# Kernel tuning notes

Hardware: AMD Instinct MI355X
Metric: run time of the kernel (lower is better)

## Reference

```python
import jax, jax.numpy as jnp
import numpy as np

B, N, M = 16, 4096, 1024
C2, C1 = 256, 128          # points2 channels (in_channel), points1 channels
MLP = [256, 256]
IN0 = C2 + C1              # use_points1=True concat


def setup_inputs() -> dict:
    key = jax.random.key(0)
    ks = jax.random.split(key, 8)
    inp = {
        "xyz1": jax.random.normal(ks[0], (B, 3, N), jnp.float32),
        "xyz2": jax.random.normal(ks[1], (B, 3, M), jnp.float32),
        "points1": jax.random.normal(ks[2], (B, C1, N), jnp.float32),
        "points2": jax.random.normal(ks[3], (B, C2, M), jnp.float32),
        # 1x1 Conv1d weights == dense matrices (out, in)
        "W1": jax.random.normal(ks[4], (MLP[0], IN0), jnp.float32) / np.sqrt(IN0),
        "b1": jnp.zeros((MLP[0],), jnp.float32),
        "W2": jax.random.normal(ks[5], (MLP[1], MLP[0]), jnp.float32) / np.sqrt(MLP[0]),
        "b2": jnp.zeros((MLP[1],), jnp.float32),
    }
    return inp


def _fp(xyz1, xyz2, points1, points2, W1, b1, W2, b2):
    # three_nn: squared pairwise distances via ||a||^2 + ||b||^2 - 2 a.b
    # xyz*: (B, 3, N/M)
    sq1 = jnp.sum(xyz1 * xyz1, axis=1)                 # (B, N)
    sq2 = jnp.sum(xyz2 * xyz2, axis=1)                 # (B, M)
    inner = jnp.einsum("bcn,bcm->bnm", xyz1, xyz2)     # (B, N, M)
    d2 = sq1[:, :, None] + sq2[:, None, :] - 2.0 * inner
    neg_d2, idx = jax.lax.top_k(-d2, 3)                # 3 smallest -> (B, N, 3)
    dist = jnp.sqrt(jnp.maximum(-neg_d2, 1e-20))       # Euclidean, like three_nn wrapper
    dist = jnp.maximum(dist, 1e-10)                    # torch.clamp_min
    recip = 1.0 / dist
    weight = recip / jnp.sum(recip, axis=2, keepdims=True)  # (B, N, 3)
    # three_interpolate: gather points2 at idx and weighted-sum
    gathered = jax.vmap(lambda p, i: p[:, i])(points2, idx)  # (B, C2, N, 3)
    interp = jnp.einsum("bcnk,bnk->bcn", gathered, weight)   # (B, C2, N)
    x = jnp.concatenate([interp, points1], axis=1)           # (B, C2+C1, N)
    # mlp_conv: 1x1 conv + relu (if_bn=False)
    x = jax.nn.relu(jnp.einsum("oc,bcn->bon", W1, x) + b1[None, :, None])
    x = jax.nn.relu(jnp.einsum("oc,bcn->bon", W2, x) + b2[None, :, None])
    return x


def reference(xyz1, xyz2, points1, points2, W1, b1, W2, b2):
    return _fp(xyz1, xyz2, points1, points2, W1, b1, W2, b2)
```

## Files before the change

### kernel.cpp

```cpp
#include <hip/hip_runtime.h>

#define B_  16
#define N_  4096
#define M_  1024
#define C1_ 128
#define C2_ 256
#define K0_ 384
#define O1_ 256
#define O2_ 256

typedef _Float16 half4  __attribute__((ext_vector_type(4)));
typedef _Float16 half8  __attribute__((ext_vector_type(8)));
typedef float    f32x4  __attribute__((ext_vector_type(4)));

__global__ __launch_bounds__(256)
void three_nn_kernel(const float* __restrict__ xyz1, const float* __restrict__ xyz2,
                     int* __restrict__ idxb, float* __restrict__ wb) {
    __shared__ float pts[4 * 1028];
    int b = blockIdx.y;
    int t = threadIdx.x;
    {
        const float* src = xyz2 + (size_t)b * 3 * M_;
        int m0 = t * 4;
        f32x4 xv = *(const f32x4*)(src + m0);
        f32x4 yv = *(const f32x4*)(src + M_ + m0);
        f32x4 zv = *(const f32x4*)(src + 2 * M_ + m0);
        float* dst = pts + (t >> 6) * 1028 + (m0 & 255) * 4;
#pragma unroll
        for (int jj = 0; jj < 4; ++jj) {
            f32x4 o = {xv[jj], yv[jj], zv[jj],
                       fmaf(xv[jj], xv[jj], fmaf(yv[jj], yv[jj], zv[jj] * zv[jj]))};
            *(f32x4*)(dst + jj * 4) = o;
        }
    }
    __syncthreads();
    int lane = t & 63;
    int c = lane & 3;
    int q = ((t >> 6) << 4) + (lane >> 2);
    int n = blockIdx.x * 64 + q;
    const float* qp = xyz1 + (size_t)b * 3 * N_;
    float px = qp[n], py = qp[N_ + n], pz = qp[2 * N_ + n];
    float px2 = -2.f * px, py2 = -2.f * py, pz2 = -2.f * pz;
    const float* base = pts + c * 1028;
    float b0 = 1e30f, b1v = 1e30f, b2v = 1e30f;
    int i0 = 0, i1 = 0, i2 = 0;
    int mb = c * 256;
#pragma unroll 4
    for (int i = 0; i < 256; ++i) {
        f32x4 pv = *(const f32x4*)(base + i * 4);
        float d = fmaf(pv[0], px2, fmaf(pv[1], py2, fmaf(pv[2], pz2, pv[3])));
        int m = mb + i;
        bool c0 = d < b0, c1 = d < b1v, c2 = d < b2v;
        float nb1 = __builtin_amdgcn_fmed3f(d, b0, b1v);
        float nb2 = __builtin_amdgcn_fmed3f(d, b1v, b2v);
        i2 = c1 ? i1 : (c2 ? m : i2);
        i1 = c0 ? i0 : (c1 ? m : i1);
        i0 = c0 ? m : i0;
        b0 = fminf(b0, d);
        b1v = nb1; b2v = nb2;
    }
#pragma unroll
    for (int st = 1; st <= 2; st <<= 1) {
        float d0 = __shfl_xor(b0, st, 64);  int j0 = __shfl_xor(i0, st, 64);
        float d1 = __shfl_xor(b1v, st, 64); int j1 = __shfl_xor(i1, st, 64);
        float d2 = __shfl_xor(b2v, st, 64); int j2 = __shfl_xor(i2, st, 64);
#pragma unroll
        for (int e = 0; e < 3; ++e) {
            float d = (e == 0) ? d0 : (e == 1) ? d1 : d2;
            int   m = (e == 0) ? j0 : (e == 1) ? j1 : j2;
            bool c0 = d < b0, c1 = d < b1v, c2 = d < b2v;
            float nb1 = __builtin_amdgcn_fmed3f(d, b0, b1v);
            float nb2 = __builtin_amdgcn_fmed3f(d, b1v, b2v);
            i2 = c1 ? i1 : (c2 ? m : i2);
            i1 = c0 ? i0 : (c1 ? m : i1);
            i0 = c0 ? m : i0;
            b0 = fminf(b0, d);
            b1v = nb1; b2v = nb2;
        }
    }
    if (c == 0) {
        float sq1 = fmaf(px, px, fmaf(py, py, pz * pz));
        float e0 = fmaxf(sqrtf(fmaxf(b0 + sq1, 1e-20f)), 1e-10f);
        float e1 = fmaxf(sqrtf(fmaxf(b1v + sq1, 1e-20f)), 1e-10f);
        float e2 = fmaxf(sqrtf(fmaxf(b2v + sq1, 1e-20f)), 1e-10f);
        float r0 = 1.f / e0, r1 = 1.f / e1, r2 = 1.f / e2;
        float s = r0 + r1 + r2;
        size_t j = ((size_t)b * N_ + n) * 3;
        idxb[j] = i0; idxb[j + 1] = i1; idxb[j + 2] = i2;
        wb[j] = r0 / s; wb[j + 1] = r1 / s; wb[j + 2] = r2 / s;
    }
}

__global__ __launch_bounds__(256)
void convert_w_kernel(const float* __restrict__ W1, const float* __restrict__ W2,
                      _Float16* __restrict__ W1h, _Float16* __restrict__ W2h) {
    int t = blockIdx.x * 256 + threadIdx.x;
    if (t < O1_ * K0_) W1h[t] = (_Float16)W1[t];
    if (t < O2_ * O1_) W2h[t] = (_Float16)W2[t];
}

__global__ __launch_bounds__(256)
void transpose_f16_kernel(const float* __restrict__ in, _Float16* __restrict__ out) {
    __shared__ float tile[64][65];
    int t = threadIdx.x;
    int nb = blockIdx.x * 64, cb = blockIdx.y * 64;
    const float* ib = in + (size_t)blockIdx.z * C2_ * M_;
#pragma unroll
    for (int r = 0; r < 16; ++r) {
        int cc = r * 4 + (t >> 6);
        tile[cc][t & 63] = ib[(size_t)(cb + cc) * M_ + nb + (t & 63)];
    }
    __syncthreads();
    _Float16* ob = out + (size_t)blockIdx.z * M_ * C2_;
#pragma unroll
    for (int pass = 0; pass < 2; ++pass) {
        int id = pass * 256 + t;
        int nl = id >> 3;
        int c8 = (id & 7) * 8;
        half8 v;
#pragma unroll
        for (int jj = 0; jj < 8; ++jj) v[jj] = (_Float16)tile[c8 + jj][nl];
        *(half8*)(ob + (size_t)(nb + nl) * C2_ + cb + c8) = v;
    }
}

__global__ __launch_bounds__(256, 2)
void fused_mlp_kernel(const _Float16* __restrict__ p2T, const int* __restrict__ idxb,
                      const float* __restrict__ wb, const float* __restrict__ points1,
                      const _Float16* __restrict__ W1h, const float* __restrict__ b1,
                      const _Float16* __restrict__ W2h, const float* __restrict__ b2,
                      float* __restrict__ out) {
    __shared__ _Float16 Y1s[128 * 256];
    char* ybase = (char*)Y1s;
    int b = blockIdx.y;
    int n0b = blockIdx.x * 128;
    int t = threadIdx.x, lane = t & 63, wv = t >> 6;
    int lr = lane & 15, lh = lane >> 4;
    int wvn = wv >> 1, wvo = wv & 1;
    int swz = (lr & 7) << 4;

    int ia[4], ib_[4], ic[4];
    float wa[4], wbv[4], wcv[4];
    const _Float16* p2b = p2T + (size_t)b * M_ * C2_;
#pragma unroll
    for (int nf = 0; nf < 4; ++nf) {
        int n = n0b + wvn * 64 + nf * 16 + lr;
        size_t j = ((size_t)b * N_ + n) * 3;
        ia[nf] = idxb[j]; ib_[nf] = idxb[j + 1]; ic[nf] = idxb[j + 2];
        wa[nf] = wb[j]; wbv[nf] = wb[j + 1]; wcv[nf] = wb[j + 2];
    }

    f32x4 acc[8][4];
#pragma unroll
    for (int of = 0; of < 8; ++of) {
        int o = wvo * 128 + of * 16 + lh * 4;
        f32x4 bv = {b1[o], b1[o + 1], b1[o + 2], b1[o + 3]};
#pragma unroll
        for (int nf = 0; nf < 4; ++nf) acc[of][nf] = bv;
    }
    const _Float16* w1p = W1h + (size_t)(wvo * 128 + lr) * K0_ + lh * 8;

    for (int k0 = 0; k0 < 256; k0 += 32) {
        half8 bf[4];
#pragma unroll
        for (int nf = 0; nf < 4; ++nf) {
            const _Float16* g0 = p2b + (size_t)ia[nf]  * C2_ + k0 + lh * 8;
            const _Float16* g1 = p2b + (size_t)ib_[nf] * C2_ + k0 + lh * 8;
            const _Float16* g2 = p2b + (size_t)ic[nf]  * C2_ + k0 + lh * 8;
            half8 va = *(const half8*)g0, vb = *(const half8*)g1, vc = *(const half8*)g2;
#pragma unroll
            for (int jj = 0; jj < 8; ++jj) {
                float v = wa[nf] * (float)va[jj] + wbv[nf] * (float)vb[jj]
                        + wcv[nf] * (float)vc[jj];
                bf[nf][jj] = (_Float16)v;
            }
        }
#pragma unroll
        for (int of = 0; of < 8; ++of) {
            half8 af = *(const half8*)(w1p + (size_t)of * 16 * K0_ + k0);
#pragma unroll
            for (int nf = 0; nf < 4; ++nf)
                acc[of][nf] = __builtin_amdgcn_mfma_f32_16x16x32_f16(af, bf[nf], acc[of][nf], 0, 0, 0);
        }
    }
    for (int k0 = 0; k0 < 128; k0 += 32) {
        half8 bf[4];
#pragma unroll
        for (int nf = 0; nf < 4; ++nf) {
            int n = n0b + wvn * 64 + nf * 16 + lr;
            const float* pp = points1 + ((size_t)b * C1_ + k0 + lh * 8) * N_ + n;
#pragma unroll
            for (int jj = 0; jj < 8; ++jj) bf[nf][jj] = (_Float16)pp[(size_t)jj * N_];
        }
#pragma unroll
        for (int of = 0; of < 8; ++of) {
            half8 af = *(const half8*)(w1p + (size_t)of * 16 * K0_ + 256 + k0);
#pragma unroll
            for (int nf = 0; nf < 4; ++nf)
                acc[of][nf] = __builtin_amdgcn_mfma_f32_16x16x32_f16(af, bf[nf], acc[of][nf], 0, 0, 0);
        }
    }
#pragma unroll
    for (int of = 0; of < 8; ++of) {
#pragma unroll
        for (int nf = 0; nf < 4; ++nf) {
            int nloc = wvn * 64 + nf * 16 + lr;
            int obyte = (wvo * 128 + of * 16 + lh * 4) * 2;
            half4 h;
#pragma unroll
            for (int r = 0; r < 4; ++r) h[r] = (_Float16)fmaxf(acc[of][nf][r], 0.f);
            *(half4*)(ybase + ((nloc * 512 + obyte) ^ swz)) = h;
        }
    }
    __syncthreads();

    f32x4 acc2[4][8];
    int o2b = wv * 64;
#pragma unroll
    for (int of = 0; of < 4; ++of) {
        int o = o2b + of * 16 + lh * 4;
        f32x4 bv = {b2[o], b2[o + 1], b2[o + 2], b2[o + 3]};
#pragma unroll
        for (int nf = 0; nf < 8; ++nf) acc2[of][nf] = bv;
    }
    const _Float16* w2p = W2h + (size_t)(o2b + lr) * O1_ + lh * 8;
    for (int k0 = 0; k0 < 256; k0 += 32) {
        half8 av[4];
#pragma unroll
        for (int of = 0; of < 4; ++of) av[of] = *(const half8*)(w2p + (size_t)of * 16 * O1_ + k0);
#pragma unroll
        for (int nf = 0; nf < 8; ++nf) {
            half8 bb = *(const half8*)(ybase + ((((nf * 16 + lr) * 512) + k0 * 2 + lh * 16) ^ swz));
#pragma unroll
            for (int of = 0; of < 4; ++of)
                acc2[of][nf] = __builtin_amdgcn_mfma_f32_16x16x32_f16(av[of], bb, acc2[of][nf], 0, 0, 0);
        }
    }
    float* ob = out + (size_t)b * O2_ * N_;
#pragma unroll
    for (int of = 0; of < 4; ++of) {
#pragma unroll
        for (int r = 0; r < 4; ++r) {
            int o2 = o2b + of * 16 + lh * 4 + r;
#pragma unroll
            for (int nf = 0; nf < 8; ++nf)
                ob[(size_t)o2 * N_ + n0b + nf * 16 + lr] = fmaxf(acc2[of][nf][r], 0.f);
        }
    }
}

extern "C" void kernel_launch(void* const* d_in, const int* in_sizes, int n_in,
                              void* d_out, int out_size, void* d_ws, size_t ws_size,
                              hipStream_t stream) {
    const float* xyz1    = (const float*)d_in[0];
    const float* xyz2    = (const float*)d_in[1];
    const float* points1 = (const float*)d_in[2];
    const float* points2 = (const float*)d_in[3];
    const float* W1      = (const float*)d_in[4];
    const float* b1      = (const float*)d_in[5];
    const float* W2      = (const float*)d_in[6];
    const float* b2      = (const float*)d_in[7];
    float* out = (float*)d_out;

    char* p = (char*)d_ws;
    auto alloc = [&](size_t bytes) -> char* {
        char* r = p;
        p += (bytes + 255) & ~(size_t)255;
        return r;
    };
    _Float16* W1h  = (_Float16*)alloc((size_t)O1_ * K0_ * 2);
    _Float16* W2h  = (_Float16*)alloc((size_t)O2_ * O1_ * 2);
    int*      idxb = (int*)alloc((size_t)B_ * N_ * 3 * 4);
    float*    wbuf = (float*)alloc((size_t)B_ * N_ * 3 * 4);
    _Float16* p2T  = (_Float16*)alloc((size_t)B_ * M_ * C2_ * 2);
    (void)ws_size;

    convert_w_kernel<<<dim3((O1_ * K0_ + 255) / 256), 256, 0, stream>>>(W1, W2, W1h, W2h);
    three_nn_kernel<<<dim3(N_ / 64, B_), 256, 0, stream>>>(xyz1, xyz2, idxb, wbuf);
    transpose_f16_kernel<<<dim3(M_ / 64, C2_ / 64, B_), 256, 0, stream>>>(points2, p2T);
    fused_mlp_kernel<<<dim3(N_ / 128, B_), 256, 0, stream>>>(
        p2T, idxb, wbuf, points1, W1h, b1, W2h, b2, out);
}
```

Measured before the change: 202.5 us.

## Stage interpolated features in LDS, retile MLP to 64-point blocks, pre-transpose points1

The fused MLP kernel now gathers and interpolates the points2 features once into swizzled shared memory, then runs both 1x1-conv GEMMs from LDS. It uses 512-thread blocks over 64 points with smaller per-wave accumulators, which allows higher occupancy. points1 is optionally transposed to fp16 first when the workspace is large enough, so it can be read with vector loads instead of strided scalar loads. three_nn now splits each query across 8 lanes with half the candidate range per lane and runs twice as many blocks. In exchange there is an extra transpose pass over points1 and a larger dynamic shared memory footprint.

```diff
diff --git a/kernel.cpp b/kernel.cpp
--- a/kernel.cpp
+++ b/kernel.cpp
@@ -16,7 +16,7 @@
 __global__ __launch_bounds__(256)
 void three_nn_kernel(const float* __restrict__ xyz1, const float* __restrict__ xyz2,
                      int* __restrict__ idxb, float* __restrict__ wb) {
-    __shared__ float pts[4 * 1028];
+    __shared__ float pts[8 * 516];
     int b = blockIdx.y;
     int t = threadIdx.x;
     {
@@ -25,7 +25,7 @@
         f32x4 xv = *(const f32x4*)(src + m0);
         f32x4 yv = *(const f32x4*)(src + M_ + m0);
         f32x4 zv = *(const f32x4*)(src + 2 * M_ + m0);
-        float* dst = pts + (t >> 6) * 1028 + (m0 & 255) * 4;
+        float* dst = pts + (m0 >> 7) * 516 + (m0 & 127) * 4;
 #pragma unroll
         for (int jj = 0; jj < 4; ++jj) {
             f32x4 o = {xv[jj], yv[jj], zv[jj],
@@ -35,18 +35,18 @@
     }
     __syncthreads();
     int lane = t & 63;
-    int c = lane & 3;
-    int q = ((t >> 6) << 4) + (lane >> 2);
-    int n = blockIdx.x * 64 + q;
+    int c = lane & 7;
+    int q = ((t >> 6) << 3) + (lane >> 3);
+    int n = blockIdx.x * 32 + q;
     const float* qp = xyz1 + (size_t)b * 3 * N_;
     float px = qp[n], py = qp[N_ + n], pz = qp[2 * N_ + n];
     float px2 = -2.f * px, py2 = -2.f * py, pz2 = -2.f * pz;
-    const float* base = pts + c * 1028;
+    const float* base = pts + c * 516;
     float b0 = 1e30f, b1v = 1e30f, b2v = 1e30f;
     int i0 = 0, i1 = 0, i2 = 0;
-    int mb = c * 256;
+    int mb = c * 128;
 #pragma unroll 4
-    for (int i = 0; i < 256; ++i) {
+    for (int i = 0; i < 128; ++i) {
         f32x4 pv = *(const f32x4*)(base + i * 4);
         float d = fmaf(pv[0], px2, fmaf(pv[1], py2, fmaf(pv[2], pz2, pv[3])));
         int m = mb + i;
@@ -60,7 +60,7 @@
         b1v = nb1; b2v = nb2;
     }
 #pragma unroll
-    for (int st = 1; st <= 2; st <<= 1) {
+    for (int st = 1; st <= 4; st <<= 1) {
         float d0 = __shfl_xor(b0, st, 64);  int j0 = __shfl_xor(i0, st, 64);
         float d1 = __shfl_xor(b1v, st, 64); int j1 = __shfl_xor(i1, st, 64);
         float d2 = __shfl_xor(b2v, st, 64); int j2 = __shfl_xor(i2, st, 64);
@@ -78,7 +78,7 @@
             b1v = nb1; b2v = nb2;
         }
     }
-    if (c == 0) {
+    if ((lane & 7) == 0) {
         float sq1 = fmaf(px, px, fmaf(py, py, pz * pz));
         float e0 = fmaxf(sqrtf(fmaxf(b0 + sq1, 1e-20f)), 1e-10f);
         float e1 = fmaxf(sqrtf(fmaxf(b1v + sq1, 1e-20f)), 1e-10f);
@@ -100,18 +100,20 @@
 }
 
 __global__ __launch_bounds__(256)
-void transpose_f16_kernel(const float* __restrict__ in, _Float16* __restrict__ out) {
+void transpose_f16_kernel(const float* __restrict__ in, _Float16* __restrict__ out,
+                          int NP, size_t in_bstride, size_t out_bstride,
+                          int out_rstride) {
     __shared__ float tile[64][65];
     int t = threadIdx.x;
     int nb = blockIdx.x * 64, cb = blockIdx.y * 64;
-    const float* ib = in + (size_t)blockIdx.z * C2_ * M_;
+    const float* ib = in + blockIdx.z * in_bstride;
 #pragma unroll
     for (int r = 0; r < 16; ++r) {
         int cc = r * 4 + (t >> 6);
-        tile[cc][t & 63] = ib[(size_t)(cb + cc) * M_ + nb + (t & 63)];
+        tile[cc][t & 63] = ib[(size_t)(cb + cc) * NP + nb + (t & 63)];
     }
     __syncthreads();
-    _Float16* ob = out + (size_t)blockIdx.z * M_ * C2_;
+    _Float16* ob = out + blockIdx.z * out_bstride;
 #pragma unroll
     for (int pass = 0; pass < 2; ++pass) {
         int id = pass * 256 + t;
@@ -120,131 +122,137 @@
         half8 v;
 #pragma unroll
         for (int jj = 0; jj < 8; ++jj) v[jj] = (_Float16)tile[c8 + jj][nl];
-        *(half8*)(ob + (size_t)(nb + nl) * C2_ + cb + c8) = v;
-    }
-}
-
-__global__ __launch_bounds__(256, 2)
+        *(half8*)(ob + (size_t)(nb + nl) * out_rstride + cb + c8) = v;
+    }
+}
+
+__global__ __launch_bounds__(512, 4)
 void fused_mlp_kernel(const _Float16* __restrict__ p2T, const int* __restrict__ idxb,
                       const float* __restrict__ wb, const float* __restrict__ points1,
+                      const _Float16* __restrict__ p1T,
                       const _Float16* __restrict__ W1h, const float* __restrict__ b1,
                       const _Float16* __restrict__ W2h, const float* __restrict__ b2,
                       float* __restrict__ out) {
-    __shared__ _Float16 Y1s[128 * 256];
-    char* ybase = (char*)Y1s;
+    extern __shared__ char smem[];
+    char* Xs = smem;
+    char* Ys = smem + 64 * 768;
     int b = blockIdx.y;
-    int n0b = blockIdx.x * 128;
+    int n0b = blockIdx.x * 64;
     int t = threadIdx.x, lane = t & 63, wv = t >> 6;
     int lr = lane & 15, lh = lane >> 4;
-    int wvn = wv >> 1, wvo = wv & 1;
-    int swz = (lr & 7) << 4;
-
-    int ia[4], ib_[4], ic[4];
-    float wa[4], wbv[4], wcv[4];
-    const _Float16* p2b = p2T + (size_t)b * M_ * C2_;
-#pragma unroll
-    for (int nf = 0; nf < 4; ++nf) {
-        int n = n0b + wvn * 64 + nf * 16 + lr;
-        size_t j = ((size_t)b * N_ + n) * 3;
-        ia[nf] = idxb[j]; ib_[nf] = idxb[j + 1]; ic[nf] = idxb[j + 2];
-        wa[nf] = wb[j]; wbv[nf] = wb[j + 1]; wcv[nf] = wb[j + 2];
-    }
-
-    f32x4 acc[8][4];
-#pragma unroll
-    for (int of = 0; of < 8; ++of) {
-        int o = wvo * 128 + of * 16 + lh * 4;
+
+    {
+        int row = t >> 3, seg = t & 7;
+        size_t j = ((size_t)b * N_ + n0b + row) * 3;
+        int i0 = idxb[j], i1 = idxb[j + 1], i2 = idxb[j + 2];
+        float w0 = wb[j], w1 = wb[j + 1], w2 = wb[j + 2];
+        const _Float16* pb = p2T + (size_t)b * M_ * C2_;
+        const half8* q0 = (const half8*)(pb + (size_t)i0 * C2_ + seg * 32);
+        const half8* q1 = (const half8*)(pb + (size_t)i1 * C2_ + seg * 32);
+        const half8* q2 = (const half8*)(pb + (size_t)i2 * C2_ + seg * 32);
+        half8 a0[4] = {q0[0], q0[1], q0[2], q0[3]};
+        half8 a1[4] = {q1[0], q1[1], q1[2], q1[3]};
+        half8 a2[4] = {q2[0], q2[1], q2[2], q2[3]};
+        int rswz = (row & 7) << 4;
+        char* xrow = Xs + row * 768;
+#pragma unroll
+        for (int x = 0; x < 4; ++x) {
+            half8 v;
+#pragma unroll
+            for (int jj = 0; jj < 8; ++jj)
+                v[jj] = (_Float16)(w0 * (float)a0[x][jj] + w1 * (float)a1[x][jj]
+                                 + w2 * (float)a2[x][jj]);
+            *(half8*)(xrow + ((seg * 64 + x * 16) ^ rswz)) = v;
+        }
+        if (p1T) {
+            const half8* q3 = (const half8*)(p1T + ((size_t)b * N_ + n0b + row) * C1_ + seg * 16);
+            half8 c0v = q3[0], c1v = q3[1];
+            *(half8*)(xrow + ((512 + seg * 32) ^ rswz)) = c0v;
+            *(half8*)(xrow + ((512 + seg * 32 + 16) ^ rswz)) = c1v;
+        } else {
+            const float* pp = points1 + ((size_t)b * C1_ + seg * 16) * N_ + n0b + row;
+            half8 c0v, c1v;
+#pragma unroll
+            for (int jj = 0; jj < 8; ++jj) c0v[jj] = (_Float16)pp[(size_t)jj * N_];
+#pragma unroll
+            for (int jj = 0; jj < 8; ++jj) c1v[jj] = (_Float16)pp[(size_t)(8 + jj) * N_];
+            *(half8*)(xrow + ((512 + seg * 32) ^ rswz)) = c0v;
+            *(half8*)(xrow + ((512 + seg * 32 + 16) ^ rswz)) = c1v;
+        }
+    }
+    __syncthreads();
+
+    int wvo = wv & 3, wvn = wv >> 2;
+    int r0 = wvn * 32 + lr;
+    int swz = (r0 & 7) << 4;
+    char* x0 = Xs + r0 * 768;
+    char* x1 = x0 + 16 * 768;
+
+    f32x4 acc[4][2];
+#pragma unroll
+    for (int of = 0; of < 4; ++of) {
+        int o = wvo * 64 + of * 16 + lh * 4;
         f32x4 bv = {b1[o], b1[o + 1], b1[o + 2], b1[o + 3]};
-#pragma unroll
-        for (int nf = 0; nf < 4; ++nf) acc[of][nf] = bv;
-    }
-    const _Float16* w1p = W1h + (size_t)(wvo * 128 + lr) * K0_ + lh * 8;
-
-    for (int k0 = 0; k0 < 256; k0 += 32) {
-        half8 bf[4];
-#pragma unroll
-        for (int nf = 0; nf < 4; ++nf) {
-            const _Float16* g0 = p2b + (size_t)ia[nf]  * C2_ + k0 + lh * 8;
-            const _Float16* g1 = p2b + (size_t)ib_[nf] * C2_ + k0 + lh * 8;
-            const _Float16* g2 = p2b + (size_t)ic[nf]  * C2_ + k0 + lh * 8;
-            half8 va = *(const half8*)g0, vb = *(const half8*)g1, vc = *(const half8*)g2;
-#pragma unroll
-            for (int jj = 0; jj < 8; ++jj) {
-                float v = wa[nf] * (float)va[jj] + wbv[nf] * (float)vb[jj]
-                        + wcv[nf] * (float)vc[jj];
-                bf[nf][jj] = (_Float16)v;
+        acc[of][0] = bv; acc[of][1] = bv;
+    }
+    const _Float16* w1p = W1h + (size_t)(wvo * 64 + lr) * K0_ + lh * 8;
+#pragma unroll
+    for (int k0 = 0; k0 < K0_; k0 += 32) {
+        half8 bf0 = *(const half8*)(x0 + ((k0 * 2 + lh * 16) ^ swz));
+        half8 bf1 = *(const half8*)(x1 + ((k0 * 2 + lh * 16) ^ swz));
+#pragma unroll
+        for (int of = 0; of < 4; ++of) {
+            half8 af = *(const half8*)(w1p + (size_t)of * 16 * K0_ + k0);
+            acc[of][0] = __builtin_amdgcn_mfma_f32_16x16x32_f16(af, bf0, acc[of][0], 0, 0, 0);
+            acc[of][1] = __builtin_amdgcn_mfma_f32_16x16x32_f16(af, bf1, acc[of][1], 0, 0, 0);
+        }
+    }
+#pragma unroll
+    for (int of = 0; of < 4; ++of) {
+#pragma unroll
+        for (int nf = 0; nf < 2; ++nf) {
+            int nrow = wvn * 32 + nf * 16 + lr;
+            int obyte = (wvo * 64 + of * 16 + lh * 4) * 2;
+            half4 h;
+#pragma unroll
+            for (int r = 0; r < 4; ++r) h[r] = (_Float16)fmaxf(acc[of][nf][r], 0.f);
+            *(half4*)(Ys + ((nrow * 512 + obyte) ^ ((nrow & 7) << 4))) = h;
+        }
+    }
+    __syncthreads();
+
+    f32x4 acc2[4][2];
+#pragma unroll
+    for (int of = 0; of < 4; ++of) {
+        int o = wvo * 64 + of * 16 + lh * 4;
+        f32x4 bv = {b2[o], b2[o + 1], b2[o + 2], b2[o + 3]};
+        acc2[of][0] = bv; acc2[of][1] = bv;
+    }
+    const _Float16* w2p = W2h + (size_t)(wvo * 64 + lr) * O1_ + lh * 8;
+    char* y0 = Ys + r0 * 512;
+    char* y1 = y0 + 16 * 512;
+#pragma unroll
+    for (int k0 = 0; k0 < O1_; k0 += 32) {
+        half8 bb0 = *(const half8*)(y0 + ((k0 * 2 + lh * 16) ^ swz));
+        half8 bb1 = *(const half8*)(y1 + ((k0 * 2 + lh * 16) ^ swz));
+#pragma unroll
+        for (int of = 0; of < 4; ++of) {
+            half8 af = *(const half8*)(w2p + (size_t)of * 16 * O1_ + k0);
+            acc2[of][0] = __builtin_amdgcn_mfma_f32_16x16x32_f16(af, bb0, acc2[of][0], 0, 0, 0);
+            acc2[of][1] = __builtin_amdgcn_mfma_f32_16x16x32_f16(af, bb1, acc2[of][1], 0, 0, 0);
+        }
+    }
+    float* ob = out + (size_t)b * O2_ * N_;
+#pragma unroll
+    for (int of = 0; of < 4; ++of) {
+#pragma unroll
+        for (int r = 0; r < 4; ++r) {
+            int o2 = wvo * 64 + of * 16 + lh * 4 + r;
+#pragma unroll
+            for (int nf = 0; nf < 2; ++nf) {
+                int n = n0b + wvn * 32 + nf * 16 + lr;
+                ob[(size_t)o2 * N_ + n] = fmaxf(acc2[of][nf][r], 0.f);
             }
-        }
-#pragma unroll
-        for (int of = 0; of < 8; ++of) {
-            half8 af = *(const half8*)(w1p + (size_t)of * 16 * K0_ + k0);
-#pragma unroll
-            for (int nf = 0; nf < 4; ++nf)
-                acc[of][nf] = __builtin_amdgcn_mfma_f32_16x16x32_f16(af, bf[nf], acc[of][nf], 0, 0, 0);
-        }
-    }
-    for (int k0 = 0; k0 < 128; k0 += 32) {
-        half8 bf[4];
-#pragma unroll
-        for (int nf = 0; nf < 4; ++nf) {
-            int n = n0b + wvn * 64 + nf * 16 + lr;
-            const float* pp = points1 + ((size_t)b * C1_ + k0 + lh * 8) * N_ + n;
-#pragma unroll
-            for (int jj = 0; jj < 8; ++jj) bf[nf][jj] = (_Float16)pp[(size_t)jj * N_];
-        }
-#pragma unroll
-        for (int of = 0; of < 8; ++of) {
-            half8 af = *(const half8*)(w1p + (size_t)of * 16 * K0_ + 256 + k0);
-#pragma unroll
-            for (int nf = 0; nf < 4; ++nf)
-                acc[of][nf] = __builtin_amdgcn_mfma_f32_16x16x32_f16(af, bf[nf], acc[of][nf], 0, 0, 0);
-        }
-    }
-#pragma unroll
-    for (int of = 0; of < 8; ++of) {
-#pragma unroll
-        for (int nf = 0; nf < 4; ++nf) {
-            int nloc = wvn * 64 + nf * 16 + lr;
-            int obyte = (wvo * 128 + of * 16 + lh * 4) * 2;
-            half4 h;
-#pragma unroll
-            for (int r = 0; r < 4; ++r) h[r] = (_Float16)fmaxf(acc[of][nf][r], 0.f);
-            *(half4*)(ybase + ((nloc * 512 + obyte) ^ swz)) = h;
-        }
-    }
-    __syncthreads();
-
-    f32x4 acc2[4][8];
-    int o2b = wv * 64;
-#pragma unroll
-    for (int of = 0; of < 4; ++of) {
-        int o = o2b + of * 16 + lh * 4;
-        f32x4 bv = {b2[o], b2[o + 1], b2[o + 2], b2[o + 3]};
-#pragma unroll
-        for (int nf = 0; nf < 8; ++nf) acc2[of][nf] = bv;
-    }
-    const _Float16* w2p = W2h + (size_t)(o2b + lr) * O1_ + lh * 8;
-    for (int k0 = 0; k0 < 256; k0 += 32) {
-        half8 av[4];
-#pragma unroll
-        for (int of = 0; of < 4; ++of) av[of] = *(const half8*)(w2p + (size_t)of * 16 * O1_ + k0);
-#pragma unroll
-        for (int nf = 0; nf < 8; ++nf) {
-            half8 bb = *(const half8*)(ybase + ((((nf * 16 + lr) * 512) + k0 * 2 + lh * 16) ^ swz));
-#pragma unroll
-            for (int of = 0; of < 4; ++of)
-                acc2[of][nf] = __builtin_amdgcn_mfma_f32_16x16x32_f16(av[of], bb, acc2[of][nf], 0, 0, 0);
-        }
-    }
-    float* ob = out + (size_t)b * O2_ * N_;
-#pragma unroll
-    for (int of = 0; of < 4; ++of) {
-#pragma unroll
-        for (int r = 0; r < 4; ++r) {
-            int o2 = o2b + of * 16 + lh * 4 + r;
-#pragma unroll
-            for (int nf = 0; nf < 8; ++nf)
-                ob[(size_t)o2 * N_ + n0b + nf * 16 + lr] = fmaxf(acc2[of][nf][r], 0.f);
         }
     }
 }
@@ -261,6 +269,7 @@
     const float* W2      = (const float*)d_in[6];
     const float* b2      = (const float*)d_in[7];
     float* out = (float*)d_out;
+    (void)in_sizes; (void)n_in; (void)out_size;
 
     char* p = (char*)d_ws;
     auto alloc = [&](size_t bytes) -> char* {
@@ -273,11 +282,19 @@
     int*      idxb = (int*)alloc((size_t)B_ * N_ * 3 * 4);
     float*    wbuf = (float*)alloc((size_t)B_ * N_ * 3 * 4);
     _Float16* p2T  = (_Float16*)alloc((size_t)B_ * M_ * C2_ * 2);
-    (void)ws_size;
+    size_t used = (size_t)(p - (char*)d_ws);
+    size_t p1T_bytes = (size_t)B_ * N_ * C1_ * 2;
+    _Float16* p1T = nullptr;
+    if (ws_size >= used + p1T_bytes)
+        p1T = (_Float16*)alloc(p1T_bytes);
 
     convert_w_kernel<<<dim3((O1_ * K0_ + 255) / 256), 256, 0, stream>>>(W1, W2, W1h, W2h);
-    three_nn_kernel<<<dim3(N_ / 64, B_), 256, 0, stream>>>(xyz1, xyz2, idxb, wbuf);
-    transpose_f16_kernel<<<dim3(M_ / 64, C2_ / 64, B_), 256, 0, stream>>>(points2, p2T);
-    fused_mlp_kernel<<<dim3(N_ / 128, B_), 256, 0, stream>>>(
-        p2T, idxb, wbuf, points1, W1h, b1, W2h, b2, out);
-}
+    three_nn_kernel<<<dim3(N_ / 32, B_), 256, 0, stream>>>(xyz1, xyz2, idxb, wbuf);
+    transpose_f16_kernel<<<dim3(M_ / 64, C2_ / 64, B_), 256, 0, stream>>>(
+        points2, p2T, M_, (size_t)C2_ * M_, (size_t)M_ * C2_, C2_);
+    if (p1T)
+        transpose_f16_kernel<<<dim3(N_ / 64, C1_ / 64, B_), 256, 0, stream>>>(
+            points1, p1T, N_, (size_t)C1_ * N_, (size_t)N_ * C1_, C1_);
+    fused_mlp_kernel<<<dim3(N_ / 64, B_), 512, 64 * 768 + 64 * 512, stream>>>(
+        p2T, idxb, wbuf, points1, p1T, W1h, b1, W2h, b2, out);
+}
```

Measured after the change: 233.8 us. +15.5%, slower.
